# Optimization experiments

Hardware: AMD Instinct MI355X
Metric: run time of the kernel (lower is better)

## Reference

```python
import jax, jax.numpy as jnp
import numpy as np
from jax import lax


def setup_inputs() -> dict:
    key = jax.random.key(0)
    k1, k2, k3, k4, k5 = jax.random.split(key, 5)
    b, c_in, c_out, h, wdim, k = 16, 256, 256, 64, 64, 3
    return {
        "x": jax.random.normal(k1, (b, c_in, h, wdim), dtype=jnp.float32),
        "w_style": jax.random.normal(k2, (b, 512), dtype=jnp.float32),
        "W": jax.random.normal(k3, (c_out, c_in, k, k), dtype=jnp.float32),
        "aff_w": jax.random.normal(k4, (c_in, 512), dtype=jnp.float32) * 0.02,
        "aff_b": jax.random.normal(k5, (c_in,), dtype=jnp.float32) * 0.02,
    }


def reference(x, w_style, W, aff_w, aff_b):
    # x: [b, c_in, h, w]; w_style: [b, 512]; W: [c_out, c_in, k, k]
    k = W.shape[-1]
    pad = k // 2
    # style modulation: s = affine(w) + 1, per-sample per-input-channel scale
    s = w_style @ aff_w.T + aff_b + 1.0                     # [b, c_in]
    wgt = W[None] * s[:, None, :, None, None]               # [b, c_out, c_in, k, k]
    # demodulation: normalize each per-sample output filter
    d = lax.rsqrt(jnp.sum(wgt * wgt, axis=(2, 3, 4)) + 1e-8)  # [b, c_out]
    wgt = wgt * d[:, :, None, None, None]
    # per-sample conv (math-equivalent to the groups=b grouped-conv trick)
    def conv_one(xi, wi):
        # xi: [c_in, h, w], wi: [c_out, c_in, k, k]
        return lax.conv_general_dilated(
            xi[None], wi,
            window_strides=(1, 1),
            padding=[(pad, pad), (pad, pad)],
            dimension_numbers=("NCHW", "OIHW", "NCHW"),
        )[0]
    return jax.vmap(conv_one)(x, wgt)                       # [b, c_out, h, w]
```

## Files before the change

### kernel.cpp

```cpp
#include <hip/hip_runtime.h>
#include <hip/hip_bf16.h>

#define BATCH 16
#define CIN   256
#define COUT  256
#define HH    64
#define WW    64
#define SDIM  512
#define NPIX  4096
#define PADH  66
#define PADW  66

typedef __hip_bfloat16 bf16;
typedef __attribute__((ext_vector_type(8))) short short8;
typedef __attribute__((ext_vector_type(4))) float f32x4;

__device__ __forceinline__ void glds16(const void* g, void* l) {
    __builtin_amdgcn_global_load_lds(
        (const __attribute__((address_space(1))) unsigned int*)g,
        (__attribute__((address_space(3))) unsigned int*)l, 16, 0, 0);
}

__global__ __launch_bounds__(256) void style_kernel(
    const float* __restrict__ w_style, const float* __restrict__ aff_w,
    const float* __restrict__ aff_b, float* __restrict__ s)
{
    const int b = blockIdx.x, c = threadIdx.x;
    __shared__ float ws[SDIM];
    for (int j = c; j < SDIM; j += 256) ws[j] = w_style[b * SDIM + j];
    __syncthreads();
    const float* aw = aff_w + (size_t)c * SDIM;
    float acc = 0.f;
#pragma unroll 4
    for (int j = 0; j < SDIM; j += 4) {
        const float4 a = *(const float4*)(aw + j);
        acc += a.x * ws[j] + a.y * ws[j + 1] + a.z * ws[j + 2] + a.w * ws[j + 3];
    }
    s[b * CIN + c] = acc + aff_b[c] + 1.0f;
}

__global__ __launch_bounds__(256) void prep_kernel(
    const float* __restrict__ W, const float* __restrict__ s,
    const float* __restrict__ x,
    bf16* __restrict__ wt, bf16* __restrict__ xt)
{
    __shared__ union {
        float wl[CIN * 9];
        bf16  t[WW][CIN + 2];
        float red4[4];
    } sh;
    const int tid = threadIdx.x;

    if (blockIdx.x < BATCH * COUT) {
        const int bc = blockIdx.x, b = bc >> 8, co = bc & 255, ci = tid;
        const float* wrow = W + (size_t)co * (CIN * 9);
        for (int i = ci; i < CIN * 9 / 4; i += 256)
            *(float4*)&sh.wl[i * 4] = *(const float4*)(wrow + i * 4);
        __syncthreads();
        const float sv = s[b * CIN + ci];
        float m[9], part = 0.f;
#pragma unroll
        for (int r = 0; r < 9; ++r) { m[r] = sh.wl[ci * 9 + r] * sv; part += m[r] * m[r]; }
#pragma unroll
        for (int off = 32; off > 0; off >>= 1)
            part += __shfl_down(part, off, 64);
        __syncthreads();
        __shared__ float red[4];
        if ((ci & 63) == 0) red[ci >> 6] = part;
        __syncthreads();
        const float d = rsqrtf(red[0] + red[1] + red[2] + red[3] + 1e-8f);
#pragma unroll
        for (int r = 0; r < 9; ++r)
            wt[(((size_t)b * 9 + r) * COUT + co) * CIN + ci] = __float2bfloat16(m[r] * d);
    } else {
        const int xb  = blockIdx.x - BATCH * COUT;
        const int row = xb % PADH, b = xb / PADH;
        bf16* orow = xt + (((size_t)b * PADH + row) * PADW) * CIN;

        if (row == 0 || row == PADH - 1) {
            const uint4 z = {0, 0, 0, 0};
            for (int i = tid; i < PADW * CIN / 8; i += 256) ((uint4*)orow)[i] = z;
            return;
        }
        const float* xr = x + ((size_t)b * CIN * NPIX) + (size_t)(row - 1) * WW;
        for (int i = tid; i < CIN * (WW / 4); i += 256) {
            const int ci = i >> 4, c4 = (i & 15) * 4;
            const float4 v = *(const float4*)(xr + (size_t)ci * NPIX + c4);
            sh.t[c4 + 0][ci] = __float2bfloat16(v.x);
            sh.t[c4 + 1][ci] = __float2bfloat16(v.y);
            sh.t[c4 + 2][ci] = __float2bfloat16(v.z);
            sh.t[c4 + 3][ci] = __float2bfloat16(v.w);
        }
        __syncthreads();
        for (int i = tid; i < PADW * (CIN / 8); i += 256) {
            const int col = i >> 5, c8 = (i & 31) * 8;
            uint4 v = {0, 0, 0, 0};
            if (col > 0 && col < PADW - 1) {
                const unsigned* tp = (const unsigned*)&sh.t[col - 1][c8];
                v.x = tp[0]; v.y = tp[1]; v.z = tp[2]; v.w = tp[3];
            }
            ((uint4*)orow)[i] = v;
        }
    }
}

__global__ __launch_bounds__(256) void gemm_kernel(
    const bf16* __restrict__ xt,
    const bf16* __restrict__ wt,
    float* __restrict__ out)
{
    const int bid = blockIdx.x;
    const int b  = bid >> 6;
    const int mt = (bid >> 5) & 1;
    const int nt = bid & 31;
    const int tid  = threadIdx.x;
    const int wave = tid >> 6, lane = tid & 63;
    const int wm = wave >> 1, wn = wave & 1;
    const int lm = lane & 15, quad = lane >> 4;

    __shared__ bf16 Ash[128 * 64];
    __shared__ bf16 Bsh[4 * PADW * 64];

    f32x4 acc[4][4] = {};

    const int y0 = nt * 2;
    const bf16* xb = xt + (size_t)b * PADH * PADW * CIN;
    const bf16* wb = wt + ((size_t)b * 9) * COUT * CIN + (size_t)mt * 128 * CIN;

    int pyl[4], pxx[4];
#pragma unroll
    for (int ni = 0; ni < 4; ++ni) {
        const int px = wn * 64 + ni * 16 + lm;
        pyl[ni] = px >> 6; pxx[ni] = px & 63;
    }

    for (int ci0 = 0; ci0 < CIN; ci0 += 64) {
        __syncthreads();
        for (int i = tid; i < 4 * PADW * 8; i += 256) {
            const int row = i / (PADW * 8);
            const int j   = i - row * (PADW * 8);
            const int col = j >> 3, pc = j & 7;
            const int p   = row * PADW + col;
            const int lc  = pc ^ (p & 7);
            glds16(xb + (((size_t)(y0 + row) * PADW + col) * CIN + ci0 + lc * 8),
                   Bsh + i * 8);
        }
#pragma unroll 1
        for (int r = 0; r < 9; ++r) {
            if (r) __syncthreads();
            const bf16* wr = wb + r * (COUT * CIN) + ci0;
            for (int i = tid; i < 1024; i += 256) {
                const int co = i >> 3, pc = i & 7;
                const int lc = pc ^ (co & 7);
                glds16(wr + co * CIN + lc * 8, Ash + i * 8);
            }
            __syncthreads();

            const int dy = r / 3 - 1, dx = r % 3 - 1;
#pragma unroll
            for (int kk = 0; kk < 2; ++kk) {
                short8 af[4], bfr[4];
#pragma unroll
                for (int mi = 0; mi < 4; ++mi) {
                    const int arow = wm * 64 + mi * 16 + lm;
                    const int lc   = kk * 4 + quad;
                    af[mi] = *(const short8*)(Ash + arow * 64
                                              + (lc ^ (arow & 7)) * 8);
                }
#pragma unroll
                for (int ni = 0; ni < 4; ++ni) {
                    const int p  = (1 + pyl[ni] + dy) * PADW + pxx[ni] + 1 + dx;
                    const int lc = kk * 4 + quad;
                    bfr[ni] = *(const short8*)(Bsh + p * 64
                                               + (lc ^ (p & 7)) * 8);
                }
#pragma unroll
                for (int mi = 0; mi < 4; ++mi)
#pragma unroll
                    for (int ni = 0; ni < 4; ++ni)
                        acc[mi][ni] = __builtin_amdgcn_mfma_f32_16x16x32_bf16(
                            af[mi], bfr[ni], acc[mi][ni], 0, 0, 0);
            }
        }
    }

    float* ob = out + (size_t)b * COUT * NPIX + (size_t)mt * 128 * NPIX + nt * 128;
#pragma unroll
    for (int mi = 0; mi < 4; ++mi) {
        const int cl = wm * 64 + mi * 16 + quad * 4;
#pragma unroll
        for (int ni = 0; ni < 4; ++ni) {
            const int px = wn * 64 + ni * 16 + lm;
#pragma unroll
            for (int v = 0; v < 4; ++v)
                ob[(size_t)(cl + v) * NPIX + px] = acc[mi][ni][v];
        }
    }
}

template <bool FUSE_S>
__global__ __launch_bounds__(256) void conv_mod_kernel(
    const float* __restrict__ x, const float* __restrict__ W,
    const float* __restrict__ s_pre, const float* __restrict__ w_style,
    const float* __restrict__ aff_w, const float* __restrict__ aff_b,
    float* __restrict__ out)
{
    const int bc = blockIdx.x, b = bc >> 8, co = bc & 255, tid = threadIdx.x;
    __shared__ float wsh[CIN * 9];
    __shared__ float red[CIN];
    float sv;
    if (FUSE_S) {
        __shared__ float wst[SDIM];
        for (int j = tid; j < SDIM; j += 256) wst[j] = w_style[b * SDIM + j];
        __syncthreads();
        const float* aw = aff_w + tid * SDIM;
        float a2 = 0.f;
#pragma unroll 8
        for (int j = 0; j < SDIM; ++j) a2 += wst[j] * aw[j];
        sv = a2 + aff_b[tid] + 1.0f;
    } else sv = s_pre[b * CIN + tid];
    {
        const float* wp = W + (co * CIN + tid) * 9;
        float m[9], part = 0.f;
#pragma unroll
        for (int r = 0; r < 9; ++r) { m[r] = wp[r] * sv; part += m[r] * m[r]; }
        red[tid] = part;
        __syncthreads();
#pragma unroll
        for (int off = CIN / 2; off > 0; off >>= 1) {
            if (tid < off) red[tid] += red[tid + off];
            __syncthreads();
        }
        const float d = rsqrtf(red[0] + 1e-8f);
#pragma unroll
        for (int r = 0; r < 9; ++r) wsh[tid * 9 + r] = m[r] * d;
        __syncthreads();
    }
    const int p = blockIdx.y * 256 + tid, y = p >> 6, xx = p & 63;
    const bool vt = y > 0, vb = y < HH - 1, vl = xx > 0, vr = xx < WW - 1;
    const bool val[9] = { vt && vl, vt, vt && vr, vl, true, vr, vb && vl, vb, vb && vr };
    const int off9[9] = { -WW - 1, -WW, -WW + 1, -1, 0, 1, WW - 1, WW, WW + 1 };
    const float* xbp = x + (size_t)b * CIN * NPIX + p;
    float acc = 0.f;
    for (int ci = 0; ci < CIN; ++ci) {
        const float* xp = xbp + ci * NPIX;
        const float* wp = wsh + ci * 9;
#pragma unroll
        for (int r = 0; r < 9; ++r) acc += (val[r] ? xp[off9[r]] : 0.f) * wp[r];
    }
    out[(size_t)bc * NPIX + p] = acc;
}

extern "C" void kernel_launch(void* const* d_in, const int* in_sizes, int n_in,
                              void* d_out, int out_size, void* d_ws, size_t ws_size,
                              hipStream_t stream) {
    const float* x       = (const float*)d_in[0];
    const float* w_style = (const float*)d_in[1];
    const float* W       = (const float*)d_in[2];
    const float* aff_w   = (const float*)d_in[3];
    const float* aff_b   = (const float*)d_in[4];
    float* out = (float*)d_out;

    const size_t wt_off  = 65536;
    const size_t wt_sz   = (size_t)BATCH * 9 * COUT * CIN * sizeof(bf16);
    const size_t xt_off  = wt_off + wt_sz;
    const size_t xt_sz   = (size_t)BATCH * PADH * PADW * CIN * sizeof(bf16);
    const size_t need    = xt_off + xt_sz;

    if (ws_size >= need) {
        float* s  = (float*)d_ws;
        bf16* wt  = (bf16*)((char*)d_ws + wt_off);
        bf16* xt  = (bf16*)((char*)d_ws + xt_off);
        style_kernel<<<dim3(BATCH), dim3(256), 0, stream>>>(w_style, aff_w, aff_b, s);
        prep_kernel<<<dim3(BATCH * COUT + BATCH * PADH), dim3(256), 0, stream>>>(
            W, s, x, wt, xt);
        gemm_kernel<<<dim3(BATCH * 64), dim3(256), 0, stream>>>(xt, wt, out);
    } else if (ws_size >= (size_t)(BATCH * CIN * sizeof(float))) {
        float* s = (float*)d_ws;
        style_kernel<<<dim3(BATCH), dim3(256), 0, stream>>>(w_style, aff_w, aff_b, s);
        conv_mod_kernel<false><<<dim3(BATCH * COUT, NPIX / 256), dim3(256), 0, stream>>>(
            x, W, s, w_style, aff_w, aff_b, out);
    } else {
        conv_mod_kernel<true><<<dim3(BATCH * COUT, NPIX / 256), dim3(256), 0, stream>>>(
            x, W, nullptr, w_style, aff_w, aff_b, out);
    }
}
```

Baseline: 228.8 us.

## Double-buffer weight tiles and prefetch next tap during MFMA compute

Splits the weight shared-memory tile into two buffers. The next filter tap's weights are fetched with global_load_lds while the current tap's MFMAs run, and the next input-channel activation slab is loaded after the last tap's fragments are already in registers. This removes one barrier and the exposed global-load latency per tap, at the cost of an extra 16KB of LDS per block, which may reduce occupancy. It also wraps the MFMA block in s_setprio so the wave doing math keeps priority.

```diff
diff --git a/kernel.cpp b/kernel.cpp
--- a/kernel.cpp
+++ b/kernel.cpp
@@ -118,7 +118,7 @@
     const int wm = wave >> 1, wn = wave & 1;
     const int lm = lane & 15, quad = lane >> 4;
 
-    __shared__ bf16 Ash[128 * 64];
+    __shared__ bf16 Ash[2][128 * 64];
     __shared__ bf16 Bsh[4 * PADW * 64];
 
     f32x4 acc[4][4] = {};
@@ -127,59 +127,103 @@
     const bf16* xb = xt + (size_t)b * PADH * PADW * CIN;
     const bf16* wb = wt + ((size_t)b * 9) * COUT * CIN + (size_t)mt * 128 * CIN;
 
-    int pyl[4], pxx[4];
+    int p0[4];
 #pragma unroll
     for (int ni = 0; ni < 4; ++ni) {
         const int px = wn * 64 + ni * 16 + lm;
-        pyl[ni] = px >> 6; pxx[ni] = px & 63;
-    }
-
-    for (int ci0 = 0; ci0 < CIN; ci0 += 64) {
-        __syncthreads();
-        for (int i = tid; i < 4 * PADW * 8; i += 256) {
-            const int row = i / (PADW * 8);
-            const int j   = i - row * (PADW * 8);
-            const int col = j >> 3, pc = j & 7;
-            const int p   = row * PADW + col;
-            const int lc  = pc ^ (p & 7);
-            glds16(xb + (((size_t)(y0 + row) * PADW + col) * CIN + ci0 + lc * 8),
-                   Bsh + i * 8);
-        }
+        p0[ni] = (1 + (px >> 6)) * PADW + (px & 63) + 1;
+    }
+
+    for (int i = tid; i < 4 * PADW * 8; i += 256) {
+        const int row = i / (PADW * 8);
+        const int j   = i - row * (PADW * 8);
+        const int col = j >> 3, pc = j & 7;
+        const int p   = row * PADW + col;
+        const int lc  = pc ^ (p & 7);
+        glds16(xb + (((size_t)(y0 + row) * PADW + col) * CIN + lc * 8), Bsh + i * 8);
+    }
+#pragma unroll
+    for (int k = 0; k < 4; ++k) {
+        const int i = tid + k * 256;
+        const int co = i >> 3, pc = i & 7;
+        const int lc = pc ^ (co & 7);
+        glds16(wb + co * CIN + lc * 8, Ash[0] + i * 8);
+    }
+    __syncthreads();
+
+    int cur = 0;
+#pragma unroll 1
+    for (int c = 0; c < 4; ++c) {
+        const int ci0 = c * 64;
 #pragma unroll 1
         for (int r = 0; r < 9; ++r) {
-            if (r) __syncthreads();
-            const bf16* wr = wb + r * (COUT * CIN) + ci0;
-            for (int i = tid; i < 1024; i += 256) {
-                const int co = i >> 3, pc = i & 7;
-                const int lc = pc ^ (co & 7);
-                glds16(wr + co * CIN + lc * 8, Ash + i * 8);
-            }
-            __syncthreads();
+            if (r < 8) {
+                const bf16* wr = wb + (size_t)(r + 1) * (COUT * CIN) + ci0;
+#pragma unroll
+                for (int k = 0; k < 4; ++k) {
+                    const int i = tid + k * 256;
+                    const int co = i >> 3, pc = i & 7;
+                    const int lc = pc ^ (co & 7);
+                    glds16(wr + co * CIN + lc * 8, Ash[cur ^ 1] + i * 8);
+                }
+            }
 
             const int dy = r / 3 - 1, dx = r % 3 - 1;
+            const int dpx = dy * PADW + dx;
+
+            short8 af[2][4], bfr[2][4];
 #pragma unroll
             for (int kk = 0; kk < 2; ++kk) {
-                short8 af[4], bfr[4];
+                const int lc = kk * 4 + quad;
 #pragma unroll
                 for (int mi = 0; mi < 4; ++mi) {
                     const int arow = wm * 64 + mi * 16 + lm;
-                    const int lc   = kk * 4 + quad;
-                    af[mi] = *(const short8*)(Ash + arow * 64
-                                              + (lc ^ (arow & 7)) * 8);
+                    af[kk][mi] = *(const short8*)(Ash[cur] + arow * 64
+                                                  + (lc ^ (arow & 7)) * 8);
                 }
 #pragma unroll
                 for (int ni = 0; ni < 4; ++ni) {
-                    const int p  = (1 + pyl[ni] + dy) * PADW + pxx[ni] + 1 + dx;
-                    const int lc = kk * 4 + quad;
-                    bfr[ni] = *(const short8*)(Bsh + p * 64
-                                               + (lc ^ (p & 7)) * 8);
-                }
+                    const int p = p0[ni] + dpx;
+                    bfr[kk][ni] = *(const short8*)(Bsh + p * 64
+                                                   + (lc ^ (p & 7)) * 8);
+                }
+            }
+
+            if (r == 8 && c < 3) {
+                __syncthreads();
+                const int nci = ci0 + 64;
+                for (int i = tid; i < 4 * PADW * 8; i += 256) {
+                    const int row = i / (PADW * 8);
+                    const int j   = i - row * (PADW * 8);
+                    const int col = j >> 3, pc = j & 7;
+                    const int p   = row * PADW + col;
+                    const int lc  = pc ^ (p & 7);
+                    glds16(xb + (((size_t)(y0 + row) * PADW + col) * CIN + nci + lc * 8),
+                           Bsh + i * 8);
+                }
+#pragma unroll
+                for (int k = 0; k < 4; ++k) {
+                    const int i = tid + k * 256;
+                    const int co = i >> 3, pc = i & 7;
+                    const int lc = pc ^ (co & 7);
+                    glds16(wb + co * CIN + nci + lc * 8, Ash[cur ^ 1] + i * 8);
+                }
+            }
+
+            __builtin_amdgcn_s_setprio(1);
+#pragma unroll
+            for (int kk = 0; kk < 2; ++kk)
 #pragma unroll
                 for (int mi = 0; mi < 4; ++mi)
 #pragma unroll
                     for (int ni = 0; ni < 4; ++ni)
                         acc[mi][ni] = __builtin_amdgcn_mfma_f32_16x16x32_bf16(
-                            af[mi], bfr[ni], acc[mi][ni], 0, 0, 0);
+                            af[kk][mi], bfr[kk][ni], acc[mi][ni], 0, 0, 0);
+            __builtin_amdgcn_s_setprio(0);
+
+            if (!(r == 8 && c == 3)) {
+                __syncthreads();
+                cur ^= 1;
             }
         }
     }
```

Measured after the change: 230.5 us. Within noise of the previous version (+0.7%).

## Enlarge GEMM tile to 256x256 with double-buffered weight staging and interleaved MFMA

Applied to the files above, without the earlier changes.

The implicit-GEMM conv kernel now uses 512-thread blocks, each covering all 256 output channels and four image rows, so 256 blocks replace 1024. Weight tiles are double-buffered in LDS and the next tap's tile is prefetched while the current MFMAs run. LDS fragment reads are interleaved with MFMA groups using raw barriers and s_setprio. The aim is to cut per-tap barrier stalls and redundant input-row loads. In exchange, register and LDS use per block rise sharply, occupancy drops, and the 256-block grid may not fill all CUs.

```diff
diff --git a/kernel.cpp b/kernel.cpp
--- a/kernel.cpp
+++ b/kernel.cpp
@@ -20,6 +20,9 @@
         (const __attribute__((address_space(1))) unsigned int*)g,
         (__attribute__((address_space(3))) unsigned int*)l, 16, 0, 0);
 }
+
+#define BAR()   __builtin_amdgcn_s_barrier()
+#define VM0()   asm volatile("s_waitcnt vmcnt(0)" ::: "memory")
 
 __global__ __launch_bounds__(256) void style_kernel(
     const float* __restrict__ w_style, const float* __restrict__ aff_w,
@@ -104,90 +107,136 @@
     }
 }
 
-__global__ __launch_bounds__(256) void gemm_kernel(
+__global__ __launch_bounds__(512, 2) void gemm_kernel(
     const bf16* __restrict__ xt,
     const bf16* __restrict__ wt,
     float* __restrict__ out)
 {
     const int bid = blockIdx.x;
-    const int b  = bid >> 6;
-    const int mt = (bid >> 5) & 1;
-    const int nt = bid & 31;
+    const int b  = bid >> 4;
+    const int nt = bid & 15;
     const int tid  = threadIdx.x;
     const int wave = tid >> 6, lane = tid & 63;
-    const int wm = wave >> 1, wn = wave & 1;
+    const int wm = wave >> 2, wn = wave & 3;
     const int lm = lane & 15, quad = lane >> 4;
 
-    __shared__ bf16 Ash[128 * 64];
-    __shared__ bf16 Bsh[4 * PADW * 64];
-
-    f32x4 acc[4][4] = {};
-
-    const int y0 = nt * 2;
+    __shared__ bf16 Ash[2][256 * 64];
+    __shared__ bf16 Bsh[6 * PADW * 64];
+
+    f32x4 acc[8][4] = {};
+
     const bf16* xb = xt + (size_t)b * PADH * PADW * CIN;
-    const bf16* wb = wt + ((size_t)b * 9) * COUT * CIN + (size_t)mt * 128 * CIN;
-
-    int pyl[4], pxx[4];
-#pragma unroll
-    for (int ni = 0; ni < 4; ++ni) {
-        const int px = wn * 64 + ni * 16 + lm;
-        pyl[ni] = px >> 6; pxx[ni] = px & 63;
-    }
-
-    for (int ci0 = 0; ci0 < CIN; ci0 += 64) {
-        __syncthreads();
-        for (int i = tid; i < 4 * PADW * 8; i += 256) {
+    const bf16* wb = wt + (size_t)b * 9 * COUT * CIN;
+
+    int p0[4];
+#pragma unroll
+    for (int ni = 0; ni < 4; ++ni)
+        p0[ni] = (1 + wn) * PADW + ni * 16 + lm + 1;
+
+    auto stageA = [&](int r, int c, int buf) {
+        const bf16* wr = wb + (size_t)r * (COUT * CIN) + c * 64;
+#pragma unroll
+        for (int k = 0; k < 4; ++k) {
+            const int i = tid + k * 512;
+            const int co = i >> 3, pc = i & 7;
+            const int lc = pc ^ (co & 7);
+            glds16(wr + co * CIN + lc * 8, Ash[buf] + i * 8);
+        }
+    };
+    auto stageB = [&](int c) {
+        const int ci0 = c * 64;
+        for (int i = tid; i < 6 * PADW * 8; i += 512) {
             const int row = i / (PADW * 8);
             const int j   = i - row * (PADW * 8);
             const int col = j >> 3, pc = j & 7;
             const int p   = row * PADW + col;
             const int lc  = pc ^ (p & 7);
-            glds16(xb + (((size_t)(y0 + row) * PADW + col) * CIN + ci0 + lc * 8),
+            glds16(xb + (((size_t)(nt * 4 + row) * PADW + col) * CIN + ci0 + lc * 8),
                    Bsh + i * 8);
         }
+    };
+    auto readA = [&](short8* af, int kk, int mih, int buf) {
+#pragma unroll
+        for (int mi = 0; mi < 4; ++mi) {
+            const int arow = wm * 128 + (mih * 4 + mi) * 16 + lm;
+            const int lc   = kk * 4 + quad;
+            af[mi] = *(const short8*)(Ash[buf] + arow * 64 + (lc ^ (arow & 7)) * 8);
+        }
+    };
+    auto readB = [&](short8* bfr, int kk, int dpx) {
+#pragma unroll
+        for (int ni = 0; ni < 4; ++ni) {
+            const int p  = p0[ni] + dpx;
+            const int lc = kk * 4 + quad;
+            bfr[ni] = *(const short8*)(Bsh + p * 64 + (lc ^ (p & 7)) * 8);
+        }
+    };
+    auto mfma16 = [&](int half, const short8* af, const short8* bfr) {
+        __builtin_amdgcn_s_setprio(1);
+#pragma unroll
+        for (int mi = 0; mi < 4; ++mi)
+#pragma unroll
+            for (int ni = 0; ni < 4; ++ni)
+                acc[half * 4 + mi][ni] = __builtin_amdgcn_mfma_f32_16x16x32_bf16(
+                    af[mi], bfr[ni], acc[half * 4 + mi][ni], 0, 0, 0);
+        __builtin_amdgcn_s_setprio(0);
+    };
+
+    stageB(0);
+    stageA(0, 0, 0);
+    __syncthreads();
+
+    short8 afE[4], afO[4], bfE[4], bfO[4];
+    readA(afE, 0, 0, 0);
+    readB(bfE, 0, -PADW - 1);
+
+    int cur = 0;
+#pragma unroll 1
+    for (int c = 0; c < 4; ++c) {
 #pragma unroll 1
         for (int r = 0; r < 9; ++r) {
-            if (r) __syncthreads();
-            const bf16* wr = wb + r * (COUT * CIN) + ci0;
-            for (int i = tid; i < 1024; i += 256) {
-                const int co = i >> 3, pc = i & 7;
-                const int lc = pc ^ (co & 7);
-                glds16(wr + co * CIN + lc * 8, Ash + i * 8);
+            const bool last = (c == 3) && (r == 8);
+            const int nr = (r == 8) ? 0 : r + 1;
+            const int dpx  = (r / 3 - 1) * PADW + (r % 3 - 1);
+            const int dpxn = (nr / 3 - 1) * PADW + (nr % 3 - 1);
+
+            readA(afO, 0, 1, cur);
+            if (!last) stageA(nr, (r == 8) ? c + 1 : c, cur ^ 1);
+            BAR();
+            mfma16(0, afE, bfE);
+            BAR();
+
+            readA(afE, 1, 0, cur);
+            readB(bfO, 1, dpx);
+            BAR();
+            mfma16(1, afO, bfE);
+            BAR();
+
+            if (r == 8 && c < 3) {
+                __syncthreads();
+                stageB(c + 1);
             }
-            __syncthreads();
-
-            const int dy = r / 3 - 1, dx = r % 3 - 1;
-#pragma unroll
-            for (int kk = 0; kk < 2; ++kk) {
-                short8 af[4], bfr[4];
-#pragma unroll
-                for (int mi = 0; mi < 4; ++mi) {
-                    const int arow = wm * 64 + mi * 16 + lm;
-                    const int lc   = kk * 4 + quad;
-                    af[mi] = *(const short8*)(Ash + arow * 64
-                                              + (lc ^ (arow & 7)) * 8);
-                }
-#pragma unroll
-                for (int ni = 0; ni < 4; ++ni) {
-                    const int p  = (1 + pyl[ni] + dy) * PADW + pxx[ni] + 1 + dx;
-                    const int lc = kk * 4 + quad;
-                    bfr[ni] = *(const short8*)(Bsh + p * 64
-                                               + (lc ^ (p & 7)) * 8);
-                }
-#pragma unroll
-                for (int mi = 0; mi < 4; ++mi)
-#pragma unroll
-                    for (int ni = 0; ni < 4; ++ni)
-                        acc[mi][ni] = __builtin_amdgcn_mfma_f32_16x16x32_bf16(
-                            af[mi], bfr[ni], acc[mi][ni], 0, 0, 0);
+            readA(afO, 1, 1, cur);
+            BAR();
+            mfma16(0, afE, bfO);
+            BAR();
+
+            if (!last) VM0();
+            BAR();
+            if (!last) {
+                readA(afE, 0, 0, cur ^ 1);
+                readB(bfE, 0, dpxn);
             }
-        }
-    }
-
-    float* ob = out + (size_t)b * COUT * NPIX + (size_t)mt * 128 * NPIX + nt * 128;
-#pragma unroll
-    for (int mi = 0; mi < 4; ++mi) {
-        const int cl = wm * 64 + mi * 16 + quad * 4;
+            mfma16(1, afO, bfO);
+            BAR();
+            cur ^= 1;
+        }
+    }
+
+    float* ob = out + (size_t)b * COUT * NPIX + nt * 256;
+#pragma unroll
+    for (int mi = 0; mi < 8; ++mi) {
+        const int cl = wm * 128 + mi * 16 + quad * 4;
 #pragma unroll
         for (int ni = 0; ni < 4; ++ni) {
             const int px = wn * 64 + ni * 16 + lm;
@@ -274,7 +323,7 @@
         style_kernel<<<dim3(BATCH), dim3(256), 0, stream>>>(w_style, aff_w, aff_b, s);
         prep_kernel<<<dim3(BATCH * COUT + BATCH * PADH), dim3(256), 0, stream>>>(
             W, s, x, wt, xt);
-        gemm_kernel<<<dim3(BATCH * 64), dim3(256), 0, stream>>>(xt, wt, out);
+        gemm_kernel<<<dim3(BATCH * 16), dim3(512), 0, stream>>>(xt, wt, out);
     } else if (ws_size >= (size_t)(BATCH * CIN * sizeof(float))) {
         float* s = (float*)d_ws;
         style_kernel<<<dim3(BATCH), dim3(256), 0, stream>>>(w_style, aff_w, aff_b, s);
```

After: 221.9 us. 3.0% less time.
